# Performance work log

Measured on AMD Instinct MI355X. Metric: run time of the kernel, lower is better.

The kernel has to match this reference:

```python
import jax, jax.numpy as jnp
import numpy as np

B, L, D_IN, D_H = 8, 16384, 256, 256  # leaves L = 2**14, complete binary tree
N = 2 * L - 1  # total nodes, heap layout: children of j are 2j+1, 2j+2


def setup_inputs() -> dict:
    key = jax.random.key(0)
    ks = jax.random.split(key, 7)
    s_in = 1.0 / float(np.sqrt(D_IN))
    s_h = 1.0 / float(np.sqrt(D_H))
    return {
        "x": jax.random.normal(ks[0], (B, N, D_IN), jnp.float32),
        "W_iou": jax.random.uniform(ks[1], (D_IN, 3 * D_H), jnp.float32, -s_in, s_in),
        "b_iou": jax.random.uniform(ks[2], (3 * D_H,), jnp.float32, -s_in, s_in),
        "U_iou": jax.random.uniform(ks[3], (D_H, 3 * D_H), jnp.float32, -s_h, s_h),
        "W_f": jax.random.uniform(ks[4], (D_IN, D_H), jnp.float32, -s_in, s_in),
        "b_f": jax.random.uniform(ks[5], (D_IN,)[:0] + (D_H,), jnp.float32, -s_in, s_in),
        "U_f": jax.random.uniform(ks[6], (D_H, D_H), jnp.float32, -s_h, s_h),
    }


def reference(x, W_iou, b_iou, U_iou, W_f, b_f, U_f):
    Bn, Nn, _ = x.shape
    H = U_f.shape[0]
    Lv = (Nn + 1) // 2  # number of leaves
    depth = int(np.log2(Lv))

    # --- leaf nodes (no children): heap indices Lv-1 .. 2Lv-2 ---
    x_leaf = x[:, Lv - 1:, :]                       # [B, L, d_in]
    iou = x_leaf @ W_iou + b_iou                    # [B, L, 3H]
    i, o, u = jnp.split(iou, 3, axis=-1)
    c = jax.nn.sigmoid(i) * jnp.tanh(u)
    h = jax.nn.sigmoid(o) * jnp.tanh(c)             # [B, L, H]

    # --- internal levels, bottom-up; each node has exactly 2 children ---
    n = Lv
    for _ in range(depth):
        n //= 2
        x_lvl = x[:, n - 1:2 * n - 1, :]            # [B, n, d_in]
        hc = h.reshape(Bn, n, 2, H)                 # children hidden states
        cc = c.reshape(Bn, n, 2, H)                 # children cell states
        h_sum = hc.sum(axis=2)                      # child-sum  [B, n, H]
        iou = x_lvl @ W_iou + b_iou + h_sum @ U_iou
        i, o, u = jnp.split(iou, 3, axis=-1)
        # per-child forget gate: sigmoid(W_f x + b_f + U_f h_j)
        f = jax.nn.sigmoid((x_lvl @ W_f + b_f)[:, :, None, :]
                           + jnp.einsum('bnch,hk->bnck', hc, U_f))
        c = jax.nn.sigmoid(i) * jnp.tanh(u) + (f * cc).sum(axis=2)
        h = jax.nn.sigmoid(o) * jnp.tanh(c)

    # root h, c concatenated -> [B, 2H]
    return jnp.concatenate([h[:, 0, :], c[:, 0, :]], axis=-1)
```

## Files before the change

### kernel.cpp

```cpp
#include <hip/hip_runtime.h>
#include <math.h>


#define Bb 8
#define Lleaf 16384
#define Nn 32767
#define Dd 256

typedef __attribute__((ext_vector_type(8))) short short8;
typedef __attribute__((ext_vector_type(4))) float float4v;

__device__ __forceinline__ float sigf(float x) {
    return __builtin_amdgcn_rcpf(1.0f + __expf(-x));
}
__device__ __forceinline__ float tanh_fast(float x) {
    return fmaf(2.0f, sigf(2.0f * x), -1.0f);
}
__device__ __forceinline__ unsigned short f2bf(float f) {
    unsigned int u = __float_as_uint(f);
    u = (u + 0x7FFFu + ((u >> 16) & 1u)) >> 16;
    return (unsigned short)u;
}
__device__ __forceinline__ float bf2f(unsigned short h) {
    return __uint_as_float(((unsigned int)h) << 16);
}
__device__ __forceinline__ void load_lds16(const void* g, void* l) {
    __builtin_amdgcn_global_load_lds(
        (const __attribute__((address_space(1))) unsigned int*)g,
        (__attribute__((address_space(3))) unsigned int*)l, 16, 0, 0);
}

__global__ __launch_bounds__(256) void xcast(
    const float* __restrict__ x, unsigned short* __restrict__ xbf)
{
    const int base = (blockIdx.x * 256 + threadIdx.x) * 8;
    const float4* p = (const float4*)(x + base);
    const float4 f0 = p[0], f1 = p[1];
    union { unsigned short us[8]; uint4 v; } pk;
    pk.us[0] = f2bf(f0.x); pk.us[1] = f2bf(f0.y);
    pk.us[2] = f2bf(f0.z); pk.us[3] = f2bf(f0.w);
    pk.us[4] = f2bf(f1.x); pk.us[5] = f2bf(f1.y);
    pk.us[6] = f2bf(f1.z); pk.us[7] = f2bf(f1.w);
    *(uint4*)(xbf + base) = pk.v;
}

__global__ __launch_bounds__(256) void pack_internal(
    const float* __restrict__ W_iou, const float* __restrict__ U_iou,
    const float* __restrict__ W_f,   const float* __restrict__ U_f,
    unsigned short* __restrict__ Bt)
{
    const int idx = blockIdx.x * 256 + threadIdx.x;
    const int col = idx / 768, k = idx - col * 768;
    const int q = col / 80, rem = col - q * 80;
    const int g = rem >> 4, r = rem & 15;
    const int d = (q << 4) + r;
    const int seg = k >> 8, kk = k & 255;
    float val;
    if (g < 3) {
        val = (seg == 0) ? W_iou[kk * 768 + g * 256 + d]
                         : U_iou[kk * 768 + g * 256 + d];
    } else if (seg == 0) {
        val = W_f[kk * 256 + d];
    } else if (seg == 1) {
        val = (g == 3) ? U_f[kk * 256 + d] : 0.0f;
    } else {
        val = (g == 4) ? U_f[kk * 256 + d] : 0.0f;
    }
    Bt[idx] = f2bf(val);
}

__global__ __launch_bounds__(256) void pack_leaf(
    const float* __restrict__ W_iou, unsigned short* __restrict__ Btl)
{
    const int idx = blockIdx.x * 256 + threadIdx.x;
    const int col = idx >> 8, k = idx & 255;
    const int q = col / 48, rem = col - q * 48;
    const int g = rem >> 4, r = rem & 15;
    const int d = (q << 4) + r;
    Btl[idx] = f2bf(W_iou[k * 768 + g * 256 + d]);
}

__global__ __launch_bounds__(256, 3) void gemm_level_big(
    const unsigned short* __restrict__ xbf, const unsigned short* __restrict__ Bt,
    const float* __restrict__ b_iou, const float* __restrict__ b_f,
    unsigned short* __restrict__ h_out, float* __restrict__ c_out,
    const unsigned short* __restrict__ h_ch, const float* __restrict__ c_ch,
    int n, int lvl)
{
    __shared__ unsigned short Alds[128 * 64];
    __shared__ unsigned short Blds[160 * 64];
    const int tid  = threadIdx.x;
    const int wave = tid >> 6, lane = tid & 63;
    const int l16  = lane & 15, q4 = lane >> 4;
    const int bx   = blockIdx.x >> 3, by = blockIdx.x & 7;
    const int m0   = bx * 128;
    const int n0   = by * 160;
    const int lr   = lane >> 3;
    const int lp   = (lane & 7) ^ lr;

    const int b   = m0 >> lvl;
    const int xr0 = m0 + (n - 1) + b * (Nn - n);

    float4v acc[2][10];
    #pragma unroll
    for (int qq = 0; qq < 2; ++qq) {
        const int d = ((by * 2 + qq) << 4) + l16;
        float bv0 = b_iou[d], bv1 = b_iou[256 + d], bv2 = b_iou[512 + d];
        float bv3 = b_f[d];
        float bv[5] = {bv0, bv1, bv2, bv3, bv3};
        #pragma unroll
        for (int g = 0; g < 5; ++g) {
            float4v v; v[0] = bv[g]; v[1] = bv[g]; v[2] = bv[g]; v[3] = bv[g];
            acc[0][qq * 5 + g] = v; acc[1][qq * 5 + g] = v;
        }
    }

    for (int kk = 0; kk < 12; ++kk) {
        __syncthreads();
        #pragma unroll
        for (int it = 0; it < 4; ++it) {
            const int g = it * 4 + wave;
            const int r = g * 8 + lr;
            const unsigned short* src;
            if (kk < 4) {
                src = xbf + (((xr0 + r) << 8) + kk * 64 + lp * 8);
            } else {
                const int sel = (kk >= 8) ? 1 : 0;
                src = h_ch + (((2 * (m0 + r) + sel) << 8) + ((kk - 4) & 3) * 64 + lp * 8);
            }
            load_lds16(src, &Alds[g * 512]);
        }
        #pragma unroll
        for (int it = 0; it < 5; ++it) {
            const int g = it * 4 + wave;
            const int row = g * 8 + lr;
            load_lds16(Bt + ((n0 + row) * 768 + kk * 64 + lp * 8), &Blds[g * 512]);
        }
        __syncthreads();
        #pragma unroll
        for (int ks = 0; ks < 2; ++ks) {
            const int pa = ks * 4 + q4;
            const int sw = (pa ^ (l16 & 7)) * 8;
            const short8 a0 = *(const short8*)&Alds[(wave * 32 + l16) * 64 + sw];
            const short8 a1 = *(const short8*)&Alds[(wave * 32 + 16 + l16) * 64 + sw];
            #pragma unroll
            for (int ni = 0; ni < 10; ++ni) {
                const short8 bf = *(const short8*)&Blds[(ni * 16 + l16) * 64 + sw];
                acc[0][ni] = __builtin_amdgcn_mfma_f32_16x16x32_bf16(a0, bf, acc[0][ni], 0, 0, 0);
                acc[1][ni] = __builtin_amdgcn_mfma_f32_16x16x32_bf16(a1, bf, acc[1][ni], 0, 0, 0);
            }
        }
    }

    #pragma unroll
    for (int mi = 0; mi < 2; ++mi) {
        #pragma unroll
        for (int reg = 0; reg < 4; ++reg) {
            const int row_l = wave * 32 + mi * 16 + (q4 << 2) + reg;
            const int m = m0 + row_l;
            const int cbase = (2 * m) << 8;
            const int obase = m << 8;
            #pragma unroll
            for (int qq = 0; qq < 2; ++qq) {
                const int d = ((by * 2 + qq) << 4) + l16;
                const float i_ = acc[mi][qq * 5 + 0][reg];
                const float o_ = acc[mi][qq * 5 + 1][reg];
                const float u_ = acc[mi][qq * 5 + 2][reg];
                const float f1 = acc[mi][qq * 5 + 3][reg];
                const float f2 = acc[mi][qq * 5 + 4][reg];
                const float c1 = c_ch[cbase + d];
                const float c2 = c_ch[cbase + 256 + d];
                const float c = sigf(i_) * tanh_fast(u_) + sigf(f1) * c1 + sigf(f2) * c2;
                const float h = sigf(o_) * tanh_fast(c);
                c_out[obase + d] = c;
                h_out[obase + d] = f2bf(h);
            }
        }
    }
}

__global__ __launch_bounds__(256) void gemm_level(
    const unsigned short* __restrict__ xbf, const unsigned short* __restrict__ Bt,
    const float* __restrict__ b_iou, const float* __restrict__ b_f,
    unsigned short* __restrict__ h_out, float* __restrict__ c_out,
    const unsigned short* __restrict__ h_ch, const float* __restrict__ c_ch,
    int n, int lvl)
{
    __shared__ unsigned short Alds[128 * 64];
    __shared__ unsigned short Blds[160 * 64];
    const int tid  = threadIdx.x;
    const int wave = tid >> 6, lane = tid & 63;
    const int l16  = lane & 15, q4 = lane >> 4;
    const int m0   = blockIdx.x * 128;
    const int n0   = blockIdx.y * 160;
    const int lr   = lane >> 3;
    const int lp   = (lane & 7) ^ lr;

    float4v acc[2][10];
    #pragma unroll
    for (int qq = 0; qq < 2; ++qq) {
        const int d = ((blockIdx.y * 2 + qq) << 4) + l16;
        float bv0 = b_iou[d], bv1 = b_iou[256 + d], bv2 = b_iou[512 + d];
        float bv3 = b_f[d];
        float bv[5] = {bv0, bv1, bv2, bv3, bv3};
        #pragma unroll
        for (int g = 0; g < 5; ++g) {
            float4v v; v[0] = bv[g]; v[1] = bv[g]; v[2] = bv[g]; v[3] = bv[g];
            acc[0][qq * 5 + g] = v; acc[1][qq * 5 + g] = v;
        }
    }

    for (int kk = 0; kk < 12; ++kk) {
        __syncthreads();
        #pragma unroll
        for (int it = 0; it < 4; ++it) {
            const int g = it * 4 + wave;
            const int r = g * 8 + lr;
            const int m = m0 + r;
            const unsigned short* src;
            if (kk < 4) {
                const int b = m >> lvl;
                src = xbf + (((m + (n - 1) + b * (Nn - n)) << 8) + kk * 64 + lp * 8);
            } else {
                const int sel = (kk >= 8) ? 1 : 0;
                src = h_ch + (((2 * m + sel) << 8) + ((kk - 4) & 3) * 64 + lp * 8);
            }
            load_lds16(src, &Alds[g * 512]);
        }
        #pragma unroll
        for (int it = 0; it < 5; ++it) {
            const int g = it * 4 + wave;
            const int row = g * 8 + lr;
            load_lds16(Bt + ((n0 + row) * 768 + kk * 64 + lp * 8), &Blds[g * 512]);
        }
        __syncthreads();
        #pragma unroll
        for (int ks = 0; ks < 2; ++ks) {
            const int pa = ks * 4 + q4;
            const int sw = (pa ^ (l16 & 7)) * 8;
            const short8 a0 = *(const short8*)&Alds[(wave * 32 + l16) * 64 + sw];
            const short8 a1 = *(const short8*)&Alds[(wave * 32 + 16 + l16) * 64 + sw];
            #pragma unroll
            for (int ni = 0; ni < 10; ++ni) {
                const short8 bf = *(const short8*)&Blds[(ni * 16 + l16) * 64 + sw];
                acc[0][ni] = __builtin_amdgcn_mfma_f32_16x16x32_bf16(a0, bf, acc[0][ni], 0, 0, 0);
                acc[1][ni] = __builtin_amdgcn_mfma_f32_16x16x32_bf16(a1, bf, acc[1][ni], 0, 0, 0);
            }
        }
    }

    #pragma unroll
    for (int mi = 0; mi < 2; ++mi) {
        #pragma unroll
        for (int reg = 0; reg < 4; ++reg) {
            const int row_l = wave * 32 + mi * 16 + (q4 << 2) + reg;
            const int m = m0 + row_l;
            const int cbase = (2 * m) << 8;
            const int obase = m << 8;
            #pragma unroll
            for (int qq = 0; qq < 2; ++qq) {
                const int d = ((blockIdx.y * 2 + qq) << 4) + l16;
                const float i_ = acc[mi][qq * 5 + 0][reg];
                const float o_ = acc[mi][qq * 5 + 1][reg];
                const float u_ = acc[mi][qq * 5 + 2][reg];
                const float f1 = acc[mi][qq * 5 + 3][reg];
                const float f2 = acc[mi][qq * 5 + 4][reg];
                const float c1 = c_ch[cbase + d];
                const float c2 = c_ch[cbase + 256 + d];
                const float c = sigf(i_) * tanh_fast(u_) + sigf(f1) * c1 + sigf(f2) * c2;
                const float h = sigf(o_) * tanh_fast(c);
                c_out[obase + d] = c;
                h_out[obase + d] = f2bf(h);
            }
        }
    }
}

__global__ __launch_bounds__(256) void gemm_small(
    const unsigned short* __restrict__ xbf, const unsigned short* __restrict__ Bt,
    const float* __restrict__ b_iou, const float* __restrict__ b_f,
    unsigned short* __restrict__ h_out, float* __restrict__ c_out,
    const unsigned short* __restrict__ h_ch, const float* __restrict__ c_ch,
    int n, int lvl)
{
    __shared__ unsigned short Alds[64 * 64];
    __shared__ unsigned short Blds[160 * 64];
    const int tid  = threadIdx.x;
    const int wave = tid >> 6, lane = tid & 63;
    const int l16  = lane & 15, q4 = lane >> 4;
    const int n0   = blockIdx.y * 160;
    const int lr   = lane >> 3;
    const int lp   = (lane & 7) ^ lr;
    const int rmax = 8 * n - 1;

    float4v acc[10];
    #pragma unroll
    for (int qq = 0; qq < 2; ++qq) {
        const int d = ((blockIdx.y * 2 + qq) << 4) + l16;
        float bv0 = b_iou[d], bv1 = b_iou[256 + d], bv2 = b_iou[512 + d];
        float bv3 = b_f[d];
        float bv[5] = {bv0, bv1, bv2, bv3, bv3};
        #pragma unroll
        for (int g = 0; g < 5; ++g) {
            float4v v; v[0] = bv[g]; v[1] = bv[g]; v[2] = bv[g]; v[3] = bv[g];
            acc[qq * 5 + g] = v;
        }
    }

    for (int kk = 0; kk < 12; ++kk) {
        __syncthreads();
        #pragma unroll
        for (int it = 0; it < 2; ++it) {
            const int g = it * 4 + wave;
            const int r = g * 8 + lr;
            const int m = (r > rmax) ? rmax : r;
            const unsigned short* src;
            if (kk < 4) {
                const int b = m >> lvl;
                src = xbf + (((m + (n - 1) + b * (Nn - n)) << 8) + kk * 64 + lp * 8);
            } else {
                const int sel = (kk >= 8) ? 1 : 0;
                src = h_ch + (((2 * m + sel) << 8) + ((kk - 4) & 3) * 64 + lp * 8);
            }
            load_lds16(src, &Alds[g * 512]);
        }
        #pragma unroll
        for (int it = 0; it < 5; ++it) {
            const int g = it * 4 + wave;
            const int row = g * 8 + lr;
            load_lds16(Bt + ((n0 + row) * 768 + kk * 64 + lp * 8), &Blds[g * 512]);
        }
        __syncthreads();
        #pragma unroll
        for (int ks = 0; ks < 2; ++ks) {
            const int pa = ks * 4 + q4;
            const int sw = (pa ^ (l16 & 7)) * 8;
            const short8 a0 = *(const short8*)&Alds[(wave * 16 + l16) * 64 + sw];
            #pragma unroll
            for (int ni = 0; ni < 10; ++ni) {
                const short8 bf = *(const short8*)&Blds[(ni * 16 + l16) * 64 + sw];
                acc[ni] = __builtin_amdgcn_mfma_f32_16x16x32_bf16(a0, bf, acc[ni], 0, 0, 0);
            }
        }
    }

    #pragma unroll
    for (int reg = 0; reg < 4; ++reg) {
        const int row_l = wave * 16 + (q4 << 2) + reg;
        const int m = (row_l > rmax) ? rmax : row_l;
        const bool valid = (row_l <= rmax);
        const int cbase = (2 * m) << 8;
        const int obase = m << 8;
        #pragma unroll
        for (int qq = 0; qq < 2; ++qq) {
            const int d = ((blockIdx.y * 2 + qq) << 4) + l16;
            const float i_ = acc[qq * 5 + 0][reg];
            const float o_ = acc[qq * 5 + 1][reg];
            const float u_ = acc[qq * 5 + 2][reg];
            const float f1 = acc[qq * 5 + 3][reg];
            const float f2 = acc[qq * 5 + 4][reg];
            const float c1 = c_ch[cbase + d];
            const float c2 = c_ch[cbase + 256 + d];
            const float c = sigf(i_) * tanh_fast(u_) + sigf(f1) * c1 + sigf(f2) * c2;
            const float h = sigf(o_) * tanh_fast(c);
            if (valid) {
                c_out[obase + d] = c;
                h_out[obase + d] = f2bf(h);
            }
        }
    }
}

__global__ __launch_bounds__(256, 3) void gemm_leaf(
    const unsigned short* __restrict__ xbf, const unsigned short* __restrict__ Btl,
    const float* __restrict__ b_iou,
    unsigned short* __restrict__ h_out, float* __restrict__ c_out)
{
    __shared__ unsigned short Alds[128 * 64];
    __shared__ unsigned short Blds[96 * 64];
    const int tid  = threadIdx.x;
    const int wave = tid >> 6, lane = tid & 63;
    const int l16  = lane & 15, q4 = lane >> 4;
    const int bx   = blockIdx.x >> 3, by = blockIdx.x & 7;
    const int m0   = bx * 128;
    const int n0   = by * 96;
    const int lr   = lane >> 3;
    const int lp   = (lane & 7) ^ lr;

    const int b   = m0 >> 14;
    const int xr0 = m0 + (Lleaf - 1) + b * (Nn - Lleaf);

    float4v acc[2][6];
    #pragma unroll
    for (int qq = 0; qq < 2; ++qq) {
        const int d = ((by * 2 + qq) << 4) + l16;
        float bv[3] = {b_iou[d], b_iou[256 + d], b_iou[512 + d]};
        #pragma unroll
        for (int g = 0; g < 3; ++g) {
            float4v v; v[0] = bv[g]; v[1] = bv[g]; v[2] = bv[g]; v[3] = bv[g];
            acc[0][qq * 3 + g] = v; acc[1][qq * 3 + g] = v;
        }
    }

    for (int kk = 0; kk < 4; ++kk) {
        __syncthreads();
        #pragma unroll
        for (int it = 0; it < 4; ++it) {
            const int g = it * 4 + wave;
            const int r = g * 8 + lr;
            load_lds16(xbf + (((xr0 + r) << 8) + kk * 64 + lp * 8), &Alds[g * 512]);
        }
        #pragma unroll
        for (int it = 0; it < 3; ++it) {
            const int g = it * 4 + wave;
            const int row = g * 8 + lr;
            load_lds16(Btl + ((n0 + row) * 256 + kk * 64 + lp * 8), &Blds[g * 512]);
        }
        __syncthreads();
        #pragma unroll
        for (int ks = 0; ks < 2; ++ks) {
            const int pa = ks * 4 + q4;
            const int sw = (pa ^ (l16 & 7)) * 8;
            const short8 a0 = *(const short8*)&Alds[(wave * 32 + l16) * 64 + sw];
            const short8 a1 = *(const short8*)&Alds[(wave * 32 + 16 + l16) * 64 + sw];
            #pragma unroll
            for (int ni = 0; ni < 6; ++ni) {
                const short8 bf = *(const short8*)&Blds[(ni * 16 + l16) * 64 + sw];
                acc[0][ni] = __builtin_amdgcn_mfma_f32_16x16x32_bf16(a0, bf, acc[0][ni], 0, 0, 0);
                acc[1][ni] = __builtin_amdgcn_mfma_f32_16x16x32_bf16(a1, bf, acc[1][ni], 0, 0, 0);
            }
        }
    }

    #pragma unroll
    for (int mi = 0; mi < 2; ++mi) {
        #pragma unroll
        for (int reg = 0; reg < 4; ++reg) {
            const int row_l = wave * 32 + mi * 16 + (q4 << 2) + reg;
            const int obase = (m0 + row_l) << 8;
            #pragma unroll
            for (int qq = 0; qq < 2; ++qq) {
                const int d = ((by * 2 + qq) << 4) + l16;
                const float i_ = acc[mi][qq * 3 + 0][reg];
                const float o_ = acc[mi][qq * 3 + 1][reg];
                const float u_ = acc[mi][qq * 3 + 2][reg];
                const float c = sigf(i_) * tanh_fast(u_);
                const float h = sigf(o_) * tanh_fast(c);
                c_out[obase + d] = c;
                h_out[obase + d] = f2bf(h);
            }
        }
    }
}

__global__ __launch_bounds__(256) void out_kernel(
    const unsigned short* __restrict__ h_root, const float* __restrict__ c_root,
    float* __restrict__ out)
{
    const int t = threadIdx.x;
    const int b = blockIdx.x;
    out[b * 512 + t]       = bf2f(h_root[(b << 8) + t]);
    out[b * 512 + 256 + t] = c_root[(b << 8) + t];
}

extern "C" void kernel_launch(void* const* d_in, const int* in_sizes, int n_in,
                              void* d_out, int out_size, void* d_ws, size_t ws_size,
                              hipStream_t stream) {
    const float* x     = (const float*)d_in[0];
    const float* W_iou = (const float*)d_in[1];
    const float* b_iou = (const float*)d_in[2];
    const float* U_iou = (const float*)d_in[3];
    const float* W_f   = (const float*)d_in[4];
    const float* b_f   = (const float*)d_in[5];
    const float* U_f   = (const float*)d_in[6];
    float* out = (float*)d_out;

    char* p = (char*)d_ws;
    unsigned short* xbf = (unsigned short*)p;  p += (size_t)Bb * Nn * Dd * 2;
    float* cE = (float*)p;                     p += (size_t)Bb * Lleaf * Dd * 4;
    float* cO = (float*)p;                     p += (size_t)Bb * (Lleaf/2) * Dd * 4;
    unsigned short* hE = (unsigned short*)p;   p += (size_t)Bb * Lleaf * Dd * 2;
    unsigned short* hO = (unsigned short*)p;   p += (size_t)Bb * (Lleaf/2) * Dd * 2;
    unsigned short* Bt  = (unsigned short*)p;  p += 1280 * 768 * 2;
    unsigned short* Btl = (unsigned short*)p;

    xcast<<<(Bb * Nn * Dd) / (256 * 8), 256, 0, stream>>>(x, xbf);
    pack_internal<<<(1280 * 768) / 256, 256, 0, stream>>>(W_iou, U_iou, W_f, U_f, Bt);
    pack_leaf<<<(768 * 256) / 256, 256, 0, stream>>>(W_iou, Btl);

    gemm_leaf<<<(Bb * Lleaf / 128) * 8, 256, 0, stream>>>(xbf, Btl, b_iou, hE, cE);

    for (int lvl = 13; lvl >= 7; --lvl) {
        const int n = 1 << lvl;
        unsigned short* ho = (lvl & 1) ? hO : hE;  float* co = (lvl & 1) ? cO : cE;
        unsigned short* hc = (lvl & 1) ? hE : hO;  float* cc = (lvl & 1) ? cE : cO;
        gemm_level_big<<<(Bb * n / 128) * 8, 256, 0, stream>>>(
            xbf, Bt, b_iou, b_f, ho, co, hc, cc, n, lvl);
    }
    for (int lvl = 6; lvl >= 4; --lvl) {
        const int n = 1 << lvl;
        unsigned short* ho = (lvl & 1) ? hO : hE;  float* co = (lvl & 1) ? cO : cE;
        unsigned short* hc = (lvl & 1) ? hE : hO;  float* cc = (lvl & 1) ? cE : cO;
        gemm_level<<<dim3(Bb * n / 128, 8), 256, 0, stream>>>(
            xbf, Bt, b_iou, b_f, ho, co, hc, cc, n, lvl);
    }
    for (int lvl = 3; lvl >= 0; --lvl) {
        const int n = 1 << lvl;
        unsigned short* ho = (lvl & 1) ? hO : hE;  float* co = (lvl & 1) ? cO : cE;
        unsigned short* hc = (lvl & 1) ? hE : hO;  float* cc = (lvl & 1) ? cE : cO;
        gemm_small<<<dim3(1, 8), 256, 0, stream>>>(
            xbf, Bt, b_iou, b_f, ho, co, hc, cc, n, lvl);
    }
    out_kernel<<<Bb, 256, 0, stream>>>(hE, cE, out);
}
```

Measured before the change: 983.4 us.

## Double-buffer LDS tiles in all GEMM kernels to overlap loads with MFMA

Converts the single-buffered LDS A/B tiles in the leaf, big, generic and small level GEMM kernels into ping-pong double buffers. The next k-slice is prefetched into the alternate buffer while MFMAs consume the current one, leaving one wait plus barrier per iteration instead of two syncthreads. This doubles LDS use per block (about 72KB for the big kernels), and launch-bounds occupancy drops from 3 to 2 blocks per CU, trading latency hiding through occupancy for software pipelining.

Result: no change. 997.8 us (+1.5%).

```diff
diff --git a/kernel.cpp b/kernel.cpp
--- a/kernel.cpp
+++ b/kernel.cpp
@@ -80,15 +80,15 @@
     Btl[idx] = f2bf(W_iou[k * 768 + g * 256 + d]);
 }
 
-__global__ __launch_bounds__(256, 3) void gemm_level_big(
+__global__ __launch_bounds__(256, 2) void gemm_level_big(
     const unsigned short* __restrict__ xbf, const unsigned short* __restrict__ Bt,
     const float* __restrict__ b_iou, const float* __restrict__ b_f,
     unsigned short* __restrict__ h_out, float* __restrict__ c_out,
     const unsigned short* __restrict__ h_ch, const float* __restrict__ c_ch,
     int n, int lvl)
 {
-    __shared__ unsigned short Alds[128 * 64];
-    __shared__ unsigned short Blds[160 * 64];
+    __shared__ unsigned short Alds[2][128 * 64];
+    __shared__ unsigned short Blds[2][160 * 64];
     const int tid  = threadIdx.x;
     const int wave = tid >> 6, lane = tid & 63;
     const int l16  = lane & 15, q4 = lane >> 4;
@@ -101,22 +101,7 @@
     const int b   = m0 >> lvl;
     const int xr0 = m0 + (n - 1) + b * (Nn - n);
 
-    float4v acc[2][10];
-    #pragma unroll
-    for (int qq = 0; qq < 2; ++qq) {
-        const int d = ((by * 2 + qq) << 4) + l16;
-        float bv0 = b_iou[d], bv1 = b_iou[256 + d], bv2 = b_iou[512 + d];
-        float bv3 = b_f[d];
-        float bv[5] = {bv0, bv1, bv2, bv3, bv3};
-        #pragma unroll
-        for (int g = 0; g < 5; ++g) {
-            float4v v; v[0] = bv[g]; v[1] = bv[g]; v[2] = bv[g]; v[3] = bv[g];
-            acc[0][qq * 5 + g] = v; acc[1][qq * 5 + g] = v;
-        }
-    }
-
-    for (int kk = 0; kk < 12; ++kk) {
-        __syncthreads();
+    auto stageA = [&](int kk, unsigned short* dst) {
         #pragma unroll
         for (int it = 0; it < 4; ++it) {
             const int g = it * 4 + wave;
@@ -128,27 +113,60 @@
                 const int sel = (kk >= 8) ? 1 : 0;
                 src = h_ch + (((2 * (m0 + r) + sel) << 8) + ((kk - 4) & 3) * 64 + lp * 8);
             }
-            load_lds16(src, &Alds[g * 512]);
-        }
+            load_lds16(src, dst + g * 512);
+        }
+    };
+    auto stageB = [&](int kk, unsigned short* dst) {
         #pragma unroll
         for (int it = 0; it < 5; ++it) {
             const int g = it * 4 + wave;
             const int row = g * 8 + lr;
-            load_lds16(Bt + ((n0 + row) * 768 + kk * 64 + lp * 8), &Blds[g * 512]);
-        }
-        __syncthreads();
+            load_lds16(Bt + ((n0 + row) * 768 + kk * 64 + lp * 8), dst + g * 512);
+        }
+    };
+
+    unsigned short* Ac = Alds[0]; unsigned short* An = Alds[1];
+    unsigned short* Bc = Blds[0]; unsigned short* Bn = Blds[1];
+
+    stageA(0, Ac); stageB(0, Bc);
+
+    float4v acc[2][10];
+    #pragma unroll
+    for (int qq = 0; qq < 2; ++qq) {
+        const int d = ((by * 2 + qq) << 4) + l16;
+        float bv0 = b_iou[d], bv1 = b_iou[256 + d], bv2 = b_iou[512 + d];
+        float bv3 = b_f[d];
+        float bv[5] = {bv0, bv1, bv2, bv3, bv3};
+        #pragma unroll
+        for (int g = 0; g < 5; ++g) {
+            float4v v; v[0] = bv[g]; v[1] = bv[g]; v[2] = bv[g]; v[3] = bv[g];
+            acc[0][qq * 5 + g] = v; acc[1][qq * 5 + g] = v;
+        }
+    }
+
+    asm volatile("s_waitcnt vmcnt(0)" ::: "memory");
+    __builtin_amdgcn_s_barrier();
+
+    for (int kk = 0; kk < 12; ++kk) {
+        if (kk < 11) { stageA(kk + 1, An); stageB(kk + 1, Bn); }
         #pragma unroll
         for (int ks = 0; ks < 2; ++ks) {
             const int pa = ks * 4 + q4;
             const int sw = (pa ^ (l16 & 7)) * 8;
-            const short8 a0 = *(const short8*)&Alds[(wave * 32 + l16) * 64 + sw];
-            const short8 a1 = *(const short8*)&Alds[(wave * 32 + 16 + l16) * 64 + sw];
+            const short8 a0 = *(const short8*)&Ac[(wave * 32 + l16) * 64 + sw];
+            const short8 a1 = *(const short8*)&Ac[(wave * 32 + 16 + l16) * 64 + sw];
             #pragma unroll
             for (int ni = 0; ni < 10; ++ni) {
-                const short8 bf = *(const short8*)&Blds[(ni * 16 + l16) * 64 + sw];
+                const short8 bf = *(const short8*)&Bc[(ni * 16 + l16) * 64 + sw];
                 acc[0][ni] = __builtin_amdgcn_mfma_f32_16x16x32_bf16(a0, bf, acc[0][ni], 0, 0, 0);
                 acc[1][ni] = __builtin_amdgcn_mfma_f32_16x16x32_bf16(a1, bf, acc[1][ni], 0, 0, 0);
             }
+        }
+        if (kk < 11) {
+            asm volatile("s_waitcnt vmcnt(0)" ::: "memory");
+            __builtin_amdgcn_s_barrier();
+            unsigned short* t = Ac; Ac = An; An = t;
+            t = Bc; Bc = Bn; Bn = t;
         }
     }
 
@@ -179,15 +197,15 @@
     }
 }
 
-__global__ __launch_bounds__(256) void gemm_level(
+__global__ __launch_bounds__(256, 2) void gemm_level(
     const unsigned short* __restrict__ xbf, const unsigned short* __restrict__ Bt,
     const float* __restrict__ b_iou, const float* __restrict__ b_f,
     unsigned short* __restrict__ h_out, float* __restrict__ c_out,
     const unsigned short* __restrict__ h_ch, const float* __restrict__ c_ch,
     int n, int lvl)
 {
-    __shared__ unsigned short Alds[128 * 64];
-    __shared__ unsigned short Blds[160 * 64];
+    __shared__ unsigned short Alds[2][128 * 64];
+    __shared__ unsigned short Blds[2][160 * 64];
     const int tid  = threadIdx.x;
     const int wave = tid >> 6, lane = tid & 63;
     const int l16  = lane & 15, q4 = lane >> 4;
@@ -196,6 +214,37 @@
     const int lr   = lane >> 3;
     const int lp   = (lane & 7) ^ lr;
 
+    auto stageA = [&](int kk, unsigned short* dst) {
+        #pragma unroll
+        for (int it = 0; it < 4; ++it) {
+            const int g = it * 4 + wave;
+            const int r = g * 8 + lr;
+            const int m = m0 + r;
+            const unsigned short* src;
+            if (kk < 4) {
+                const int bb = m >> lvl;
+                src = xbf + (((m + (n - 1) + bb * (Nn - n)) << 8) + kk * 64 + lp * 8);
+            } else {
+                const int sel = (kk >= 8) ? 1 : 0;
+                src = h_ch + (((2 * m + sel) << 8) + ((kk - 4) & 3) * 64 + lp * 8);
+            }
+            load_lds16(src, dst + g * 512);
+        }
+    };
+    auto stageB = [&](int kk, unsigned short* dst) {
+        #pragma unroll
+        for (int it = 0; it < 5; ++it) {
+            const int g = it * 4 + wave;
+            const int row = g * 8 + lr;
+            load_lds16(Bt + ((n0 + row) * 768 + kk * 64 + lp * 8), dst + g * 512);
+        }
+    };
+
+    unsigned short* Ac = Alds[0]; unsigned short* An = Alds[1];
+    unsigned short* Bc = Blds[0]; unsigned short* Bn = Blds[1];
+
+    stageA(0, Ac); stageB(0, Bc);
+
     float4v acc[2][10];
     #pragma unroll
     for (int qq = 0; qq < 2; ++qq) {
@@ -210,42 +259,29 @@
         }
     }
 
+    asm volatile("s_waitcnt vmcnt(0)" ::: "memory");
+    __builtin_amdgcn_s_barrier();
+
     for (int kk = 0; kk < 12; ++kk) {
-        __syncthreads();
-        #pragma unroll
-        for (int it = 0; it < 4; ++it) {
-            const int g = it * 4 + wave;
-            const int r = g * 8 + lr;
-            const int m = m0 + r;
-            const unsigned short* src;
-            if (kk < 4) {
-                const int b = m >> lvl;
-                src = xbf + (((m + (n - 1) + b * (Nn - n)) << 8) + kk * 64 + lp * 8);
-            } else {
-                const int sel = (kk >= 8) ? 1 : 0;
-                src = h_ch + (((2 * m + sel) << 8) + ((kk - 4) & 3) * 64 + lp * 8);
-            }
-            load_lds16(src, &Alds[g * 512]);
-        }
-        #pragma unroll
-        for (int it = 0; it < 5; ++it) {
-            const int g = it * 4 + wave;
-            const int row = g * 8 + lr;
-            load_lds16(Bt + ((n0 + row) * 768 + kk * 64 + lp * 8), &Blds[g * 512]);
-        }
-        __syncthreads();
+        if (kk < 11) { stageA(kk + 1, An); stageB(kk + 1, Bn); }
         #pragma unroll
         for (int ks = 0; ks < 2; ++ks) {
             const int pa = ks * 4 + q4;
             const int sw = (pa ^ (l16 & 7)) * 8;
-            const short8 a0 = *(const short8*)&Alds[(wave * 32 + l16) * 64 + sw];
-            const short8 a1 = *(const short8*)&Alds[(wave * 32 + 16 + l16) * 64 + sw];
+            const short8 a0 = *(const short8*)&Ac[(wave * 32 + l16) * 64 + sw];
+            const short8 a1 = *(const short8*)&Ac[(wave * 32 + 16 + l16) * 64 + sw];
             #pragma unroll
             for (int ni = 0; ni < 10; ++ni) {
-                const short8 bf = *(const short8*)&Blds[(ni * 16 + l16) * 64 + sw];
+                const short8 bf = *(const short8*)&Bc[(ni * 16 + l16) * 64 + sw];
                 acc[0][ni] = __builtin_amdgcn_mfma_f32_16x16x32_bf16(a0, bf, acc[0][ni], 0, 0, 0);
                 acc[1][ni] = __builtin_amdgcn_mfma_f32_16x16x32_bf16(a1, bf, acc[1][ni], 0, 0, 0);
             }
+        }
+        if (kk < 11) {
+            asm volatile("s_waitcnt vmcnt(0)" ::: "memory");
+            __builtin_amdgcn_s_barrier();
+            unsigned short* t = Ac; Ac = An; An = t;
+            t = Bc; Bc = Bn; Bn = t;
         }
     }
 
@@ -276,15 +312,15 @@
     }
 }
 
-__global__ __launch_bounds__(256) void gemm_small(
+__global__ __launch_bounds__(256, 2) void gemm_small(
     const unsigned short* __restrict__ xbf, const unsigned short* __restrict__ Bt,
     const float* __restrict__ b_iou, const float* __restrict__ b_f,
     unsigned short* __restrict__ h_out, float* __restrict__ c_out,
     const unsigned short* __restrict__ h_ch, const float* __restrict__ c_ch,
     int n, int lvl)
 {
-    __shared__ unsigned short Alds[64 * 64];
-    __shared__ unsigned short Blds[160 * 64];
+    __shared__ unsigned short Alds[2][64 * 64];
+    __shared__ unsigned short Blds[2][160 * 64];
     const int tid  = threadIdx.x;
     const int wave = tid >> 6, lane = tid & 63;
     const int l16  = lane & 15, q4 = lane >> 4;
@@ -293,6 +329,37 @@
     const int lp   = (lane & 7) ^ lr;
     const int rmax = 8 * n - 1;
 
+    auto stageA = [&](int kk, unsigned short* dst) {
+        #pragma unroll
+        for (int it = 0; it < 2; ++it) {
+            const int g = it * 4 + wave;
+            const int r = g * 8 + lr;
+            const int m = (r > rmax) ? rmax : r;
+            const unsigned short* src;
+            if (kk < 4) {
+                const int bb = m >> lvl;
+                src = xbf + (((m + (n - 1) + bb * (Nn - n)) << 8) + kk * 64 + lp * 8);
+            } else {
+                const int sel = (kk >= 8) ? 1 : 0;
+                src = h_ch + (((2 * m + sel) << 8) + ((kk - 4) & 3) * 64 + lp * 8);
+            }
+            load_lds16(src, dst + g * 512);
+        }
+    };
+    auto stageB = [&](int kk, unsigned short* dst) {
+        #pragma unroll
+        for (int it = 0; it < 5; ++it) {
+            const int g = it * 4 + wave;
+            const int row = g * 8 + lr;
+            load_lds16(Bt + ((n0 + row) * 768 + kk * 64 + lp * 8), dst + g * 512);
+        }
+    };
+
+    unsigned short* Ac = Alds[0]; unsigned short* An = Alds[1];
+    unsigned short* Bc = Blds[0]; unsigned short* Bn = Blds[1];
+
+    stageA(0, Ac); stageB(0, Bc);
+
     float4v acc[10];
     #pragma unroll
     for (int qq = 0; qq < 2; ++qq) {
@@ -307,40 +374,27 @@
         }
     }
 
+    asm volatile("s_waitcnt vmcnt(0)" ::: "memory");
+    __builtin_amdgcn_s_barrier();
+
     for (int kk = 0; kk < 12; ++kk) {
-        __syncthreads();
-        #pragma unroll
-        for (int it = 0; it < 2; ++it) {
-            const int g = it * 4 + wave;
-            const int r = g * 8 + lr;
-            const int m = (r > rmax) ? rmax : r;
-            const unsigned short* src;
-            if (kk < 4) {
-                const int b = m >> lvl;
-                src = xbf + (((m + (n - 1) + b * (Nn - n)) << 8) + kk * 64 + lp * 8);
-            } else {
-                const int sel = (kk >= 8) ? 1 : 0;
-                src = h_ch + (((2 * m + sel) << 8) + ((kk - 4) & 3) * 64 + lp * 8);
-            }
-            load_lds16(src, &Alds[g * 512]);
-        }
-        #pragma unroll
-        for (int it = 0; it < 5; ++it) {
-            const int g = it * 4 + wave;
-            const int row = g * 8 + lr;
-            load_lds16(Bt + ((n0 + row) * 768 + kk * 64 + lp * 8), &Blds[g * 512]);
-        }
-        __syncthreads();
+        if (kk < 11) { stageA(kk + 1, An); stageB(kk + 1, Bn); }
         #pragma unroll
         for (int ks = 0; ks < 2; ++ks) {
             const int pa = ks * 4 + q4;
             const int sw = (pa ^ (l16 & 7)) * 8;
-            const short8 a0 = *(const short8*)&Alds[(wave * 16 + l16) * 64 + sw];
+            const short8 a0 = *(const short8*)&Ac[(wave * 16 + l16) * 64 + sw];
             #pragma unroll
             for (int ni = 0; ni < 10; ++ni) {
-                const short8 bf = *(const short8*)&Blds[(ni * 16 + l16) * 64 + sw];
+                const short8 bf = *(const short8*)&Bc[(ni * 16 + l16) * 64 + sw];
                 acc[ni] = __builtin_amdgcn_mfma_f32_16x16x32_bf16(a0, bf, acc[ni], 0, 0, 0);
             }
+        }
+        if (kk < 11) {
+            asm volatile("s_waitcnt vmcnt(0)" ::: "memory");
+            __builtin_amdgcn_s_barrier();
+            unsigned short* t = Ac; Ac = An; An = t;
+            t = Bc; Bc = Bn; Bn = t;
         }
     }
 
@@ -371,13 +425,13 @@
     }
 }
 
-__global__ __launch_bounds__(256, 3) void gemm_leaf(
+__global__ __launch_bounds__(256, 2) void gemm_leaf(
     const unsigned short* __restrict__ xbf, const unsigned short* __restrict__ Btl,
     const float* __restrict__ b_iou,
     unsigned short* __restrict__ h_out, float* __restrict__ c_out)
 {
-    __shared__ unsigned short Alds[128 * 64];
-    __shared__ unsigned short Blds[96 * 64];
+    __shared__ unsigned short Alds[2][128 * 64];
+    __shared__ unsigned short Blds[2][96 * 64];
     const int tid  = threadIdx.x;
     const int wave = tid >> 6, lane = tid & 63;
     const int l16  = lane & 15, q4 = lane >> 4;
@@ -390,6 +444,28 @@
     const int b   = m0 >> 14;
     const int xr0 = m0 + (Lleaf - 1) + b * (Nn - Lleaf);
 
+    auto stageA = [&](int kk, unsigned short* dst) {
+        #pragma unroll
+        for (int it = 0; it < 4; ++it) {
+            const int g = it * 4 + wave;
+            const int r = g * 8 + lr;
+            load_lds16(xbf + (((xr0 + r) << 8) + kk * 64 + lp * 8), dst + g * 512);
+        }
+    };
+    auto stageB = [&](int kk, unsigned short* dst) {
+        #pragma unroll
+        for (int it = 0; it < 3; ++it) {
+            const int g = it * 4 + wave;
+            const int row = g * 8 + lr;
+            load_lds16(Btl + ((n0 + row) * 256 + kk * 64 + lp * 8), dst + g * 512);
+        }
+    };
+
+    unsigned short* Ac = Alds[0]; unsigned short* An = Alds[1];
+    unsigned short* Bc = Blds[0]; unsigned short* Bn = Blds[1];
+
+    stageA(0, Ac); stageB(0, Bc);
+
     float4v acc[2][6];
     #pragma unroll
     for (int qq = 0; qq < 2; ++qq) {
@@ -402,33 +478,29 @@
         }
     }
 
+    asm volatile("s_waitcnt vmcnt(0)" ::: "memory");
+    __builtin_amdgcn_s_barrier();
+
     for (int kk = 0; kk < 4; ++kk) {
-        __syncthreads();
-        #pragma unroll
-        for (int it = 0; it < 4; ++it) {
-            const int g = it * 4 + wave;
-            const int r = g * 8 + lr;
-            load_lds16(xbf + (((xr0 + r) << 8) + kk * 64 + lp * 8), &Alds[g * 512]);
-        }
-        #pragma unroll
-        for (int it = 0; it < 3; ++it) {
-            const int g = it * 4 + wave;
-            const int row = g * 8 + lr;
-            load_lds16(Btl + ((n0 + row) * 256 + kk * 64 + lp * 8), &Blds[g * 512]);
-        }
-        __syncthreads();
+        if (kk < 3) { stageA(kk + 1, An); stageB(kk + 1, Bn); }
         #pragma unroll
         for (int ks = 0; ks < 2; ++ks) {
             const int pa = ks * 4 + q4;
             const int sw = (pa ^ (l16 & 7)) * 8;
-            const short8 a0 = *(const short8*)&Alds[(wave * 32 + l16) * 64 + sw];
-            const short8 a1 = *(const short8*)&Alds[(wave * 32 + 16 + l16) * 64 + sw];
+            const short8 a0 = *(const short8*)&Ac[(wave * 32 + l16) * 64 + sw];
+            const short8 a1 = *(const short8*)&Ac[(wave * 32 + 16 + l16) * 64 + sw];
             #pragma unroll
             for (int ni = 0; ni < 6; ++ni) {
-                const short8 bf = *(const short8*)&Blds[(ni * 16 + l16) * 64 + sw];
+                const short8 bf = *(const short8*)&Bc[(ni * 16 + l16) * 64 + sw];
                 acc[0][ni] = __builtin_amdgcn_mfma_f32_16x16x32_bf16(a0, bf, acc[0][ni], 0, 0, 0);
                 acc[1][ni] = __builtin_amdgcn_mfma_f32_16x16x32_bf16(a1, bf, acc[1][ni], 0, 0, 0);
             }
+        }
+        if (kk < 3) {
+            asm volatile("s_waitcnt vmcnt(0)" ::: "memory");
+            __builtin_amdgcn_s_barrier();
+            unsigned short* t = Ac; Ac = An; An = t;
+            t = Bc; Bc = Bn; Bn = t;
         }
     }
 
```
